# Kernel optimization log

Measured on AMD Instinct MI355X. Metric: run time of the kernel, lower is better.

## Reference

```python
import jax, jax.numpy as jnp
import numpy as np

NODE_DIM = 128
HIDDEN = 64
N_NODES = 2048


def setup_inputs() -> dict:
    key = jax.random.key(0)
    ks = jax.random.split(key, 7)
    s_enc = 1.0 / np.sqrt(NODE_DIM)
    s1 = 1.0 / np.sqrt(2 * HIDDEN)
    s2 = 1.0 / np.sqrt(HIDDEN)
    return {
        "node_features": jax.random.normal(ks[0], (N_NODES, NODE_DIM), dtype=jnp.float32),
        "W_enc": jax.random.uniform(ks[1], (NODE_DIM, HIDDEN), jnp.float32, -s_enc, s_enc),
        "b_enc": jax.random.uniform(ks[2], (HIDDEN,), jnp.float32, -s_enc, s_enc),
        "W1": jax.random.uniform(ks[3], (2 * HIDDEN, HIDDEN), jnp.float32, -s1, s1),
        "b1": jax.random.uniform(ks[4], (HIDDEN,), jnp.float32, -s1, s1),
        "W2": jax.random.uniform(ks[5], (HIDDEN, 1), jnp.float32, -s2, s2),
        "b2": jax.random.uniform(ks[6], (1,), jnp.float32, -s2, s2),
    }


def reference(node_features, W_enc, b_enc, W1, b1, W2, b2):
    # node encoder: (n, node_dim) -> (n, hidden)
    h = node_features @ W_enc + b_enc
    # split first edge-MLP weight into the halves acting on h_i and h_j of the concat
    Wa, Wb = W1[:HIDDEN], W1[HIDDEN:]
    a = h @ Wa  # (n, hidden) contribution from source node i
    b = h @ Wb  # (n, hidden) contribution from target node j
    # pairwise pre-activation: (n, n, hidden) == Linear(concat(h_i, h_j))
    z = jax.nn.relu(a[:, None, :] + b[None, :, :] + b1)
    logits = jnp.einsum("ijh,ho->ijo", z, W2)[..., 0] + b2[0]  # (n, n)
    T = jax.nn.sigmoid(logits)
    # diagonal is never written in the original loop -> stays 0
    n = T.shape[0]
    return T * (1.0 - jnp.eye(n, dtype=T.dtype))
```

## Files before the change

### kernel.cpp

```cpp
#include <hip/hip_runtime.h>
#include <math.h>

#define NODE_DIM 128
#define HIDDEN   64
#define NN       2048
#define LSTR     68

typedef float v2f __attribute__((ext_vector_type(2)));
typedef float v4f __attribute__((ext_vector_type(4)));

__global__ __launch_bounds__(256) void prep_kernel(
    const float* __restrict__ nf, const float* __restrict__ W_enc,
    const float* __restrict__ b_enc, const float* __restrict__ W1,
    const float* __restrict__ b1, float* __restrict__ A, float* __restrict__ BB)
{
    __shared__ float nf_s[4][NODE_DIM];
    __shared__ float h_s[4][HIDDEN];
    const int tid = threadIdx.x;
    const int rg  = tid >> 6;
    const int t   = tid & 63;
    const int r   = blockIdx.x * 4 + rg;

    ((float2*)nf_s[rg])[t] = ((const float2*)(nf + (size_t)r * NODE_DIM))[t];
    __syncthreads();

    float acc = b_enc[t];
    #pragma unroll 8
    for (int k = 0; k < NODE_DIM; ++k)
        acc = fmaf(nf_s[rg][k], W_enc[k * HIDDEN + t], acc);
    h_s[rg][t] = acc;
    __syncthreads();

    float aacc = 0.0f;
    float bacc = b1[t];
    #pragma unroll 8
    for (int k = 0; k < HIDDEN; ++k) {
        const float hv = h_s[rg][k];
        aacc = fmaf(hv, W1[k * HIDDEN + t], aacc);
        bacc = fmaf(hv, W1[(HIDDEN + k) * HIDDEN + t], bacc);
    }
    A[(size_t)r * HIDDEN + t]  = aacc;
    BB[(size_t)r * HIDDEN + t] = bacc;
}

__global__ __launch_bounds__(256, 2) void pair_kernel(
    const float* __restrict__ A, const float* __restrict__ BB,
    const float* __restrict__ W2, const float* __restrict__ b2,
    float* __restrict__ out)
{
    __shared__ __align__(16) float aL[128 * LSTR];
    __shared__ __align__(16) float bL[128 * LSTR];

    const int tid = threadIdx.x;
    const int i0  = blockIdx.y * 128;
    const int j0  = blockIdx.x * 128;

    const v4f* gA = (const v4f*)(A  + (size_t)i0 * HIDDEN);
    const v4f* gB = (const v4f*)(BB + (size_t)j0 * HIDDEN);
    #pragma unroll
    for (int k = 0; k < 8; ++k) {
        const int idx = tid + k * 256;
        const int row = idx >> 4;
        const int c   = idx & 15;
        *(v4f*)&aL[row * LSTR + c * 4] = gA[idx];
        *(v4f*)&bL[row * LSTR + c * 4] = gB[idx];
    }
    __syncthreads();

    const int ty = tid >> 4;
    const int tx = tid & 15;

    v2f acc[8][8];
    #pragma unroll
    for (int ii = 0; ii < 8; ++ii)
        #pragma unroll
        for (int jj = 0; jj < 8; ++jj)
            acc[ii][jj] = (v2f){0.0f, 0.0f};

    const v2f vz = (v2f){0.0f, 0.0f};

    #pragma unroll 2
    for (int c = 0; c < 16; ++c) {
        v4f av[8], bv[8];
        #pragma unroll
        for (int ii = 0; ii < 8; ++ii)
            av[ii] = *(const v4f*)&aL[(ty + 16 * ii) * LSTR + c * 4];
        #pragma unroll
        for (int jj = 0; jj < 8; ++jj)
            bv[jj] = *(const v4f*)&bL[(tx + 16 * jj) * LSTR + c * 4];

        const v2f w0 = (v2f){W2[c * 4 + 0], W2[c * 4 + 1]};
        const v2f w1 = (v2f){W2[c * 4 + 2], W2[c * 4 + 3]};

        #pragma unroll
        for (int ii = 0; ii < 8; ++ii) {
            const v2f a0 = __builtin_shufflevector(av[ii], av[ii], 0, 1);
            const v2f a1 = __builtin_shufflevector(av[ii], av[ii], 2, 3);
            #pragma unroll
            for (int jj = 0; jj < 8; ++jj) {
                const v2f b0 = __builtin_shufflevector(bv[jj], bv[jj], 0, 1);
                const v2f b1v = __builtin_shufflevector(bv[jj], bv[jj], 2, 3);
                v2f t0 = a0 + b0;
                t0 = __builtin_elementwise_max(t0, vz);
                acc[ii][jj] += t0 * w0;
                v2f t1 = a1 + b1v;
                t1 = __builtin_elementwise_max(t1, vz);
                acc[ii][jj] += t1 * w1;
            }
        }
    }

    const float b2v = b2[0];
    #pragma unroll
    for (int ii = 0; ii < 8; ++ii) {
        const int i = i0 + ty + 16 * ii;
        #pragma unroll
        for (int jj = 0; jj < 8; ++jj) {
            const int j = j0 + tx + 16 * jj;
            const float lg = acc[ii][jj][0] + acc[ii][jj][1] + b2v;
            const float sg = 1.0f / (1.0f + __expf(-lg));
            out[(size_t)i * NN + j] = (i == j) ? 0.0f : sg;
        }
    }
}

extern "C" void kernel_launch(void* const* d_in, const int* in_sizes, int n_in,
                              void* d_out, int out_size, void* d_ws, size_t ws_size,
                              hipStream_t stream) {
    const float* nf    = (const float*)d_in[0];
    const float* W_enc = (const float*)d_in[1];
    const float* b_enc = (const float*)d_in[2];
    const float* W1    = (const float*)d_in[3];
    const float* b1    = (const float*)d_in[4];
    const float* W2    = (const float*)d_in[5];
    const float* b2    = (const float*)d_in[6];
    float* out = (float*)d_out;

    float* A  = (float*)d_ws;
    float* BB = A + (size_t)NN * HIDDEN;

    prep_kernel<<<NN / 4, 256, 0, stream>>>(nf, W_enc, b_enc, W1, b1, A, BB);
    pair_kernel<<<dim3(NN / 128, NN / 128), 256, 0, stream>>>(
        A, BB, W2, b2, out);
}
```

Measured before the change: 100.7 us.

## Rewrite ReLU as half of x plus abs x and precompute linear terms

The pairwise MLP uses the identity relu(x) = 0.5*(x + |x|). The linear parts w·a_i and w·b_j are precomputed per node in the prep kernel, so the inner loop only accumulates w*|a+b|, where the abs can fold into the FMA as a source modifier. This removes the max operation per element but gives up packed v2f arithmetic. The pair kernel also moves to 128x64 tiles with 128 threads per block and a fully unrolled channel loop, which changes occupancy and register pressure.

```diff
diff --git a/kernel.cpp b/kernel.cpp
--- a/kernel.cpp
+++ b/kernel.cpp
@@ -12,10 +12,14 @@
 __global__ __launch_bounds__(256) void prep_kernel(
     const float* __restrict__ nf, const float* __restrict__ W_enc,
     const float* __restrict__ b_enc, const float* __restrict__ W1,
-    const float* __restrict__ b1, float* __restrict__ A, float* __restrict__ BB)
+    const float* __restrict__ b1, const float* __restrict__ W2,
+    float* __restrict__ A, float* __restrict__ BB,
+    float* __restrict__ pa, float* __restrict__ pb)
 {
     __shared__ float nf_s[4][NODE_DIM];
     __shared__ float h_s[4][HIDDEN];
+    __shared__ float ra_s[4][HIDDEN];
+    __shared__ float rb_s[4][HIDDEN];
     const int tid = threadIdx.x;
     const int rg  = tid >> 6;
     const int t   = tid & 63;
@@ -41,83 +45,99 @@
     }
     A[(size_t)r * HIDDEN + t]  = aacc;
     BB[(size_t)r * HIDDEN + t] = bacc;
+
+    const float wv = W2[t];
+    ra_s[rg][t] = wv * aacc;
+    rb_s[rg][t] = wv * bacc;
+    __syncthreads();
+
+    if (t == 0) {
+        float sa = 0.0f, sb = 0.0f;
+        #pragma unroll 8
+        for (int k = 0; k < HIDDEN; ++k) { sa += ra_s[rg][k]; sb += rb_s[rg][k]; }
+        pa[r] = sa;
+        pb[r] = sb;
+    }
 }
 
-__global__ __launch_bounds__(256, 2) void pair_kernel(
+__global__ __launch_bounds__(128) void pair_kernel(
     const float* __restrict__ A, const float* __restrict__ BB,
+    const float* __restrict__ pa, const float* __restrict__ pb,
     const float* __restrict__ W2, const float* __restrict__ b2,
     float* __restrict__ out)
 {
     __shared__ __align__(16) float aL[128 * LSTR];
-    __shared__ __align__(16) float bL[128 * LSTR];
+    __shared__ __align__(16) float bL[64 * LSTR];
 
     const int tid = threadIdx.x;
     const int i0  = blockIdx.y * 128;
-    const int j0  = blockIdx.x * 128;
+    const int j0  = blockIdx.x * 64;
 
     const v4f* gA = (const v4f*)(A  + (size_t)i0 * HIDDEN);
     const v4f* gB = (const v4f*)(BB + (size_t)j0 * HIDDEN);
     #pragma unroll
-    for (int k = 0; k < 8; ++k) {
-        const int idx = tid + k * 256;
+    for (int k = 0; k < 16; ++k) {
+        const int idx = tid + k * 128;
         const int row = idx >> 4;
         const int c   = idx & 15;
         *(v4f*)&aL[row * LSTR + c * 4] = gA[idx];
+    }
+    #pragma unroll
+    for (int k = 0; k < 8; ++k) {
+        const int idx = tid + k * 128;
+        const int row = idx >> 4;
+        const int c   = idx & 15;
         *(v4f*)&bL[row * LSTR + c * 4] = gB[idx];
     }
     __syncthreads();
 
-    const int ty = tid >> 4;
-    const int tx = tid & 15;
+    const int ty = tid >> 3;
+    const int tx = tid & 7;
 
-    v2f acc[8][8];
+    float acc[8][8] = {{0.0f}};
+
     #pragma unroll
-    for (int ii = 0; ii < 8; ++ii)
-        #pragma unroll
-        for (int jj = 0; jj < 8; ++jj)
-            acc[ii][jj] = (v2f){0.0f, 0.0f};
-
-    const v2f vz = (v2f){0.0f, 0.0f};
-
-    #pragma unroll 2
     for (int c = 0; c < 16; ++c) {
+        const float w0 = W2[c * 4 + 0];
+        const float w1 = W2[c * 4 + 1];
+        const float w2 = W2[c * 4 + 2];
+        const float w3 = W2[c * 4 + 3];
         v4f av[8], bv[8];
         #pragma unroll
         for (int ii = 0; ii < 8; ++ii)
             av[ii] = *(const v4f*)&aL[(ty + 16 * ii) * LSTR + c * 4];
         #pragma unroll
         for (int jj = 0; jj < 8; ++jj)
-            bv[jj] = *(const v4f*)&bL[(tx + 16 * jj) * LSTR + c * 4];
-
-        const v2f w0 = (v2f){W2[c * 4 + 0], W2[c * 4 + 1]};
-        const v2f w1 = (v2f){W2[c * 4 + 2], W2[c * 4 + 3]};
-
+            bv[jj] = *(const v4f*)&bL[(tx + 8 * jj) * LSTR + c * 4];
         #pragma unroll
         for (int ii = 0; ii < 8; ++ii) {
-            const v2f a0 = __builtin_shufflevector(av[ii], av[ii], 0, 1);
-            const v2f a1 = __builtin_shufflevector(av[ii], av[ii], 2, 3);
             #pragma unroll
             for (int jj = 0; jj < 8; ++jj) {
-                const v2f b0 = __builtin_shufflevector(bv[jj], bv[jj], 0, 1);
-                const v2f b1v = __builtin_shufflevector(bv[jj], bv[jj], 2, 3);
-                v2f t0 = a0 + b0;
-                t0 = __builtin_elementwise_max(t0, vz);
-                acc[ii][jj] += t0 * w0;
-                v2f t1 = a1 + b1v;
-                t1 = __builtin_elementwise_max(t1, vz);
-                acc[ii][jj] += t1 * w1;
+                const v4f t = av[ii] + bv[jj];
+                float s = acc[ii][jj];
+                s = fmaf(__builtin_fabsf(t[0]), w0, s);
+                s = fmaf(__builtin_fabsf(t[1]), w1, s);
+                s = fmaf(__builtin_fabsf(t[2]), w2, s);
+                s = fmaf(__builtin_fabsf(t[3]), w3, s);
+                acc[ii][jj] = s;
             }
         }
     }
 
     const float b2v = b2[0];
+    float par[8], pbr[8];
+    #pragma unroll
+    for (int ii = 0; ii < 8; ++ii) par[ii] = pa[i0 + ty + 16 * ii];
+    #pragma unroll
+    for (int jj = 0; jj < 8; ++jj) pbr[jj] = pb[j0 + tx + 8 * jj];
+
     #pragma unroll
     for (int ii = 0; ii < 8; ++ii) {
         const int i = i0 + ty + 16 * ii;
         #pragma unroll
         for (int jj = 0; jj < 8; ++jj) {
-            const int j = j0 + tx + 16 * jj;
-            const float lg = acc[ii][jj][0] + acc[ii][jj][1] + b2v;
+            const int j = j0 + tx + 8 * jj;
+            const float lg = fmaf(0.5f, par[ii] + pbr[jj] + acc[ii][jj], b2v);
             const float sg = 1.0f / (1.0f + __expf(-lg));
             out[(size_t)i * NN + j] = (i == j) ? 0.0f : sg;
         }
@@ -138,8 +158,11 @@
 
     float* A  = (float*)d_ws;
     float* BB = A + (size_t)NN * HIDDEN;
+    float* pa = BB + (size_t)NN * HIDDEN;
+    float* pb = pa + NN;
 
-    prep_kernel<<<NN / 4, 256, 0, stream>>>(nf, W_enc, b_enc, W1, b1, A, BB);
-    pair_kernel<<<dim3(NN / 128, NN / 128), 256, 0, stream>>>(
-        A, BB, W2, b2, out);
+    prep_kernel<<<NN / 4, 256, 0, stream>>>(nf, W_enc, b_enc, W1, b1, W2,
+                                            A, BB, pa, pb);
+    pair_kernel<<<dim3(NN / 64, NN / 128), 128, 0, stream>>>(
+        A, BB, pa, pb, W2, b2, out);
 }
```

New measurement: 109.6 us. +8.8%, slower.
